# Kernel optimization log

Hardware: AMD Instinct MI355X
Metric: run time of the kernel (lower is better)

Reference implementation:

```python
import jax, jax.numpy as jnp
import numpy as np

K = 3          # kernel size
SH, SW = 2, 1  # stride
PH, PW = 1, 1  # padding


def conv2d(x, w, b, stride, pad):
    y = jax.lax.conv_general_dilated(
        x, w, window_strides=stride,
        padding=[(pad[0], pad[0]), (pad[1], pad[1])],
        dimension_numbers=('NCHW', 'OIHW', 'NCHW'))
    return y + b[None, :, None, None]


def setup_inputs() -> dict:
    key = jax.random.key(0)
    ks = jax.random.split(key, 4)
    x = jax.random.normal(ks[0], (8, 64, 128, 128), jnp.float32)
    # scale offset weights small so sampled offsets are O(1) pixels (exercises
    # the bilinear path without sampling far out of bounds)
    w_offset = jax.random.normal(ks[1], (18, 64, 3, 3), jnp.float32) * 0.02
    b_offset = jnp.zeros((18,), jnp.float32)
    w_mask = jax.random.normal(ks[2], (9, 64, 3, 3), jnp.float32) * 0.05
    b_mask = jnp.zeros((9,), jnp.float32)
    w_conv = jax.random.normal(ks[3], (64, 64, 3, 3), jnp.float32) * (1.0 / 24.0)
    return dict(x=x, w_offset=w_offset, b_offset=b_offset,
                w_mask=w_mask, b_mask=b_mask, w_conv=w_conv)


def _bilinear_gather(x, py, px):
    # x: [B,C,H,W]; py, px: [B,K2,Ho,Wo] float sampling coordinates.
    # Zero-padding outside the image (torchvision deform_conv2d semantics).
    B, C, H, W = x.shape
    y0f = jnp.floor(py)
    x0f = jnp.floor(px)
    dy = py - y0f
    dx = px - x0f
    y0 = y0f.astype(jnp.int32)
    x0 = x0f.astype(jnp.int32)

    def corner(yi, xi, wgt):
        valid = (yi >= 0) & (yi < H) & (xi >= 0) & (xi < W)
        yc = jnp.clip(yi, 0, H - 1)
        xc = jnp.clip(xi, 0, W - 1)
        # per-batch fancy gather -> [B, C, K2, Ho, Wo]
        g = jax.vmap(lambda xb, yb, xbi: xb[:, yb, xbi])(x, yc, xc)
        return g * (wgt * valid)[:, None]

    return (corner(y0,     x0,     (1 - dy) * (1 - dx))
            + corner(y0,     x0 + 1, (1 - dy) * dx)
            + corner(y0 + 1, x0,     dy * (1 - dx))
            + corner(y0 + 1, x0 + 1, dy * dx))


def reference(x, w_offset, b_offset, w_mask, b_mask, w_conv):
    B, C, H, W = x.shape
    offset = conv2d(x, w_offset, b_offset, (SH, SW), (PH, PW))   # [B, 2*K2, Ho, Wo]
    mask = jax.nn.sigmoid(conv2d(x, w_mask, b_mask, (SH, SW), (PH, PW)))  # [B, K2, Ho, Wo]
    Ho, Wo = offset.shape[2], offset.shape[3]
    K2 = K * K
    off = offset.reshape(B, K2, 2, Ho, Wo)
    off_y = off[:, :, 0]   # [B,K2,Ho,Wo]
    off_x = off[:, :, 1]
    ky = (jnp.arange(K2) // K).astype(jnp.float32)
    kx = (jnp.arange(K2) % K).astype(jnp.float32)
    hs = (jnp.arange(Ho) * SH - PH).astype(jnp.float32)
    ws = (jnp.arange(Wo) * SW - PW).astype(jnp.float32)
    py = off_y + ky[None, :, None, None] + hs[None, None, :, None]
    px = off_x + kx[None, :, None, None] + ws[None, None, None, :]
    sampled = _bilinear_gather(x, py, px) * mask[:, None]  # [B,C,K2,Ho,Wo]
    # weighted accumulate over in-channels and kernel taps
    out = jnp.einsum('ock,bckhw->bohw', w_conv.reshape(-1, C, K2), sampled)
    return out
```

## Files before the change

### kernel.cpp

```cpp
#include <hip/hip_runtime.h>
#include <hip/hip_bf16.h>
#include <hip/hip_fp16.h>
#include <math.h>

#define BB 8
#define CC 64
#define HH 128
#define WW 128
#define HO 64
#define WO 128
#define OC 64
#define HW (HH * WW)
#define HOWO (HO * WO)

typedef __attribute__((ext_vector_type(8))) short short8;
typedef __attribute__((ext_vector_type(4))) float floatx4;

union BfBits { __hip_bfloat16 h; unsigned short s; };
__device__ __forceinline__ unsigned short f2bf(float f) {
    BfBits b; b.h = __float2bfloat16(f); return b.s;
}
__device__ __forceinline__ float bflo(unsigned int u) {
    return __uint_as_float(u << 16);
}
__device__ __forceinline__ float bfhi(unsigned int u) {
    return __uint_as_float(u & 0xFFFF0000u);
}

__global__ __launch_bounds__(256) void prep(
    const float* __restrict__ x,
    const float* __restrict__ w_off, const float* __restrict__ w_msk,
    const float* __restrict__ w_conv,
    unsigned short* __restrict__ xT, unsigned int* __restrict__ xP,
    unsigned short* __restrict__ Wom, unsigned short* __restrict__ W2)
{
    __shared__ float T[64][130];
    int tid = threadIdx.x;
    int bx = blockIdx.x;
    if (bx < 1024) {
        int b = bx & 7, y = bx >> 3;
        int wl = tid & 127, c0 = tid >> 7;
#pragma unroll
        for (int i = 0; i < 32; ++i) {
            int c = 2 * i + c0;
            T[c][wl] = x[(((size_t)b * CC + c) * HH + y) * WW + wl];
        }
        __syncthreads();
        int c = tid & 63, wg = tid >> 6;
#pragma unroll
        for (int i = 0; i < 32; ++i) {
            int wp = wg * 32 + i;
            unsigned int lo = f2bf(T[c][wp]);
            unsigned int hi = (wp < 127) ? f2bf(T[c][wp + 1]) : 0u;
            size_t e = (((size_t)b * HH + y) * WW + wp) * 64 + c;
            xT[e] = (unsigned short)lo;
            xP[e] = lo | (hi << 16);
        }
    } else if (bx < 1096) {
        int i = (bx - 1024) * 256 + tid;
        int ch = i / 576, kk = i % 576;
        int xs = kk >> 6, c = kk & 63;
        float v = 0.0f;
        if (ch < 18)      v = w_off[(ch * CC + c) * 9 + xs];
        else if (ch < 27) v = w_msk[((ch - 18) * CC + c) * 9 + xs];
        Wom[i] = f2bf(v);
    } else {
        int i = (bx - 1096) * 256 + tid;
        int k = i % 9, c = (i / 9) % CC, o = i / (CC * 9);
        W2[((size_t)k * OC + o) * CC + c] = f2bf(w_conv[i]);
    }
}

__global__ __launch_bounds__(256) void fused(
    const unsigned short* __restrict__ xT, const unsigned int* __restrict__ xP,
    const unsigned short* __restrict__ Wom, const unsigned short* __restrict__ W2,
    const float* __restrict__ b_off, const float* __restrict__ b_msk,
    float* __restrict__ out)
{
    __shared__ __align__(16) char lds[18304];
    typedef unsigned short XsRow[34][72];
    XsRow* Xs = (XsRow*)lds;
    unsigned short (*S)[32][64] = (unsigned short(*)[32][64])lds;
    uint4* meta = (uint4*)(lds + 8192);
    float (*omr)[33] = (float(*)[33])(lds + 14720);

    int tid = threadIdx.x;
    int lane = tid & 63;
    int wv = __builtin_amdgcn_readfirstlane(tid >> 6);
    int bx = blockIdx.x;
    int b = bx & 7;
    int rest = bx >> 3;
    int h = rest >> 2;
    int w0 = (rest & 3) * 32;
    int h2 = 2 * h - 1;
    int m16 = lane & 15, q = lane >> 4;

    for (int u = tid; u < 816; u += 256) {
        int ky = u / 272;
        int rem = u - ky * 272;
        int col = rem >> 3, cb = rem & 7;
        int hy = h2 + ky, wc = w0 - 1 + col;
        short8 v = {0, 0, 0, 0, 0, 0, 0, 0};
        if ((unsigned)hy < (unsigned)HH && (unsigned)wc < (unsigned)WW)
            v = *(const short8*)(xT + (((size_t)b * HH + hy) * WW + wc) * 64 + cb * 8);
        *(short8*)&Xs[ky][col][cb * 8] = v;
    }
    __syncthreads();

    {
        int mt = wv & 1, nt = wv >> 1;
        floatx4 a = (floatx4){0.f, 0.f, 0.f, 0.f};
        const unsigned short* wa = Wom + (mt * 16 + m16) * 576 + q * 8;
#pragma unroll
        for (int t = 0; t < 18; ++t) {
            int xs = t >> 1, ky = xs / 3, kx = xs % 3;
            short8 af = *(const short8*)(wa + t * 32);
            short8 bf = *(const short8*)&Xs[ky][nt * 16 + m16 + kx][(t & 1) * 32 + q * 8];
            a = __builtin_amdgcn_mfma_f32_16x16x32_bf16(af, bf, a, 0, 0, 0);
        }
#pragma unroll
        for (int r = 0; r < 4; ++r) {
            int ch = mt * 16 + q * 4 + r;
            if (ch < 27) omr[ch][nt * 16 + m16] = a[r];
        }
    }
    __syncthreads();

    for (int u = tid; u < 288; u += 256) {
        int kk = u >> 5, pos = u & 31;
        float offy = omr[2 * kk][pos] + b_off[2 * kk];
        float offx = omr[2 * kk + 1][pos] + b_off[2 * kk + 1];
        float mk = 1.0f / (1.0f + __expf(-(omr[18 + kk][pos] + b_msk[kk])));
        float py = offy + (float)(kk / 3) + (float)h2;
        float px = offx + (float)(kk % 3) + (float)(w0 + pos - 1);

        float y0f = floorf(py), x0f = floorf(px);
        float dy = py - y0f, dx = px - x0f;
        int y0 = (int)y0f, x0 = (int)x0f;
        int y1 = y0 + 1, x1 = x0 + 1;
        bool vy0 = (unsigned)y0 < (unsigned)HH;
        bool vy1 = (unsigned)y1 < (unsigned)HH;
        bool vx0 = (unsigned)x0 < (unsigned)WW;
        bool vx1 = (unsigned)x1 < (unsigned)WW;
        float w00 = (1.0f - dy) * (1.0f - dx) * ((vy0 && vx0) ? mk : 0.0f);
        float w01 = (1.0f - dy) * dx          * ((vy0 && vx1) ? mk : 0.0f);
        float w10 = dy * (1.0f - dx)          * ((vy1 && vx0) ? mk : 0.0f);
        float w11 = dy * dx                   * ((vy1 && vx1) ? mk : 0.0f);
        int xbase = min(max(x0, 0), WW - 2);
        bool s0 = x0 > xbase;
        bool s1 = x1 > xbase;
        float cxA = (s0 ? 0.f : w00) + (s1 ? 0.f : w01);
        float cyA = (s0 ? w00 : 0.f) + (s1 ? w01 : 0.f);
        float cxB = (s0 ? 0.f : w10) + (s1 ? 0.f : w11);
        float cyB = (s0 ? w10 : 0.f) + (s1 ? w11 : 0.f);
        int yc0 = min(max(y0, 0), HH - 1);
        int yc1 = min(max(y1, 0), HH - 1);

        __half2 hA = __floats2half2_rn(cxA, cyA);
        __half2 hB = __floats2half2_rn(cxB, cyB);
        uint4 mu;
        mu.x = __builtin_bit_cast(unsigned int, hA);
        mu.y = __builtin_bit_cast(unsigned int, hB);
        mu.z = (unsigned)(yc0 * WW + xbase) * 256u;
        mu.w = (unsigned)(yc1 * WW + xbase) * 256u;
        meta[u] = mu;
    }
    __syncthreads();

    int p0 = wv * 8;
    int c = lane;
    const char* xPb = (const char*)(xP + (size_t)b * HW * 64);
    floatx4 acc0 = (floatx4){0.f, 0.f, 0.f, 0.f};
    floatx4 acc1 = (floatx4){0.f, 0.f, 0.f, 0.f};

    uint4 M[8];
    unsigned int G0[8], G1[8];

    auto issue = [&](int k) {
#pragma unroll
        for (int i = 0; i < 8; ++i) {
            M[i] = meta[k * 32 + p0 + i];
            G0[i] = *(const unsigned int*)(xPb + M[i].z + 4 * c);
            G1[i] = *(const unsigned int*)(xPb + M[i].w + 4 * c);
        }
    };
    auto store = [&](int buf) {
#pragma unroll
        for (int i = 0; i < 8; ++i) {
            __half2 hA = __builtin_bit_cast(__half2, M[i].x);
            __half2 hB = __builtin_bit_cast(__half2, M[i].y);
            float v = __low2float(hA) * bflo(G0[i]) + __high2float(hA) * bfhi(G0[i])
                    + __low2float(hB) * bflo(G1[i]) + __high2float(hB) * bfhi(G1[i]);
            int pos = p0 + i;
            S[buf][pos][((c >> 3) ^ (pos & 7)) * 8 + (c & 7)] = f2bf(v);
        }
    };

    issue(0);
    store(0);

#pragma unroll
    for (int k = 0; k < 9; ++k) {
        __syncthreads();
        if (k < 8) issue(k + 1);
        {
            const unsigned short* wk = W2 + ((size_t)(k * OC) + wv * 16 + m16) * CC + q * 8;
            int buf = k & 1;
#pragma unroll
            for (int s = 0; s < 2; ++s) {
                short8 af = *(const short8*)(wk + s * 32);
                int cb = ((q + 4 * s) ^ (m16 & 7)) * 8;
                short8 bf0 = *(const short8*)&S[buf][m16][cb];
                short8 bf1 = *(const short8*)&S[buf][16 + m16][cb];
                acc0 = __builtin_amdgcn_mfma_f32_16x16x32_bf16(af, bf0, acc0, 0, 0, 0);
                acc1 = __builtin_amdgcn_mfma_f32_16x16x32_bf16(af, bf1, acc1, 0, 0, 0);
            }
        }
        if (k < 8) store((k + 1) & 1);
    }

#pragma unroll
    for (int nt = 0; nt < 2; ++nt) {
        floatx4 av = nt ? acc1 : acc0;
#pragma unroll
        for (int r = 0; r < 4; ++r) {
            int o = wv * 16 + q * 4 + r;
            out[(((size_t)b * OC + o) * HO + h) * WO + w0 + nt * 16 + m16] = av[r];
        }
    }
}

extern "C" void kernel_launch(void* const* d_in, const int* in_sizes, int n_in,
                              void* d_out, int out_size, void* d_ws, size_t ws_size,
                              hipStream_t stream)
{
    const float* x      = (const float*)d_in[0];
    const float* w_off  = (const float*)d_in[1];
    const float* b_off  = (const float*)d_in[2];
    const float* w_msk  = (const float*)d_in[3];
    const float* b_msk  = (const float*)d_in[4];
    const float* w_conv = (const float*)d_in[5];
    float* out = (float*)d_out;

    unsigned short* xT = (unsigned short*)d_ws;
    unsigned int* xP = (unsigned int*)(xT + (size_t)BB * HW * 64);
    unsigned short* Wom = (unsigned short*)(xP + (size_t)BB * HW * 64);
    unsigned short* W2 = Wom + 32 * 576;

    prep<<<dim3(1240), dim3(256), 0, stream>>>(x, w_off, w_msk, w_conv,
                                               xT, xP, Wom, W2);
    fused<<<dim3(2048), dim3(256), 0, stream>>>(xT, xP, Wom, W2,
                                                b_off, b_msk, out);
}
```

Before: 146.1 us.

## Switch to fp16 packed-pair layout with deeper gather pipelining and scalarized addresses

```diff
diff --git a/kernel.cpp b/kernel.cpp
--- a/kernel.cpp
+++ b/kernel.cpp
@@ -1,5 +1,4 @@
 #include <hip/hip_runtime.h>
-#include <hip/hip_bf16.h>
 #include <hip/hip_fp16.h>
 #include <math.h>
 
@@ -11,77 +10,95 @@
 #define WO 128
 #define OC 64
 #define HW (HH * WW)
-#define HOWO (HO * WO)
-
-typedef __attribute__((ext_vector_type(8))) short short8;
+
 typedef __attribute__((ext_vector_type(4))) float floatx4;
-
-union BfBits { __hip_bfloat16 h; unsigned short s; };
-__device__ __forceinline__ unsigned short f2bf(float f) {
-    BfBits b; b.h = __float2bfloat16(f); return b.s;
-}
-__device__ __forceinline__ float bflo(unsigned int u) {
-    return __uint_as_float(u << 16);
-}
-__device__ __forceinline__ float bfhi(unsigned int u) {
-    return __uint_as_float(u & 0xFFFF0000u);
+typedef __attribute__((ext_vector_type(8))) _Float16 half8;
+
+__device__ __forceinline__ unsigned short f2h(float f) {
+    __half h = __float2half(f);
+    return __builtin_bit_cast(unsigned short, h);
+}
+__device__ __forceinline__ unsigned int packpair(float a, float b) {
+    __half2 h = __floats2half2_rn(a, b);
+    return __builtin_bit_cast(unsigned int, h);
+}
+__device__ __forceinline__ void lgkm_barrier() {
+    asm volatile("s_waitcnt lgkmcnt(0)" ::: "memory");
+    __builtin_amdgcn_s_barrier();
 }
 
 __global__ __launch_bounds__(256) void prep(
     const float* __restrict__ x,
     const float* __restrict__ w_off, const float* __restrict__ w_msk,
     const float* __restrict__ w_conv,
-    unsigned short* __restrict__ xT, unsigned int* __restrict__ xP,
+    unsigned int* __restrict__ xP,
     unsigned short* __restrict__ Wom, unsigned short* __restrict__ W2)
 {
-    __shared__ float T[64][130];
-    int tid = threadIdx.x;
-    int bx = blockIdx.x;
-    if (bx < 1024) {
-        int b = bx & 7, y = bx >> 3;
-        int wl = tid & 127, c0 = tid >> 7;
-#pragma unroll
-        for (int i = 0; i < 32; ++i) {
-            int c = 2 * i + c0;
-            T[c][wl] = x[(((size_t)b * CC + c) * HH + y) * WW + wl];
+    __shared__ float T[64][77];
+    int tid = threadIdx.x, bx = blockIdx.x;
+    if (bx < 2048) {
+        int wh = bx & 1, b = (bx >> 1) & 7, y = bx >> 4;
+        int w0 = wh << 6;
+        const float* xb = x + (((size_t)b * CC) * HH + y) * WW + w0;
+#pragma unroll
+        for (int i = 0; i < 4; ++i) {
+            int idx = i * 256 + tid;
+            int cch = idx >> 4, f4 = (idx & 15) << 2;
+            floatx4 v = *(const floatx4*)(xb + (size_t)cch * HW + f4);
+            T[cch][f4 + 0] = v.x;
+            T[cch][f4 + 1] = v.y;
+            T[cch][f4 + 2] = v.z;
+            T[cch][f4 + 3] = v.w;
+        }
+        if (tid < 64) {
+            float e = 0.0f;
+            if (w0 + 64 < WW) e = xb[(size_t)tid * HW + 64];
+            T[tid][64] = e;
         }
         __syncthreads();
-        int c = tid & 63, wg = tid >> 6;
-#pragma unroll
-        for (int i = 0; i < 32; ++i) {
-            int wp = wg * 32 + i;
-            unsigned int lo = f2bf(T[c][wp]);
-            unsigned int hi = (wp < 127) ? f2bf(T[c][wp + 1]) : 0u;
-            size_t e = (((size_t)b * HH + y) * WW + wp) * 64 + c;
-            xT[e] = (unsigned short)lo;
-            xP[e] = lo | (hi << 16);
-        }
-    } else if (bx < 1096) {
-        int i = (bx - 1024) * 256 + tid;
-        int ch = i / 576, kk = i % 576;
-        int xs = kk >> 6, c = kk & 63;
+        int ch = tid & 63;
+        int wb = (tid >> 6) << 4;
+        size_t base = ((((size_t)b * HH + y) * WW) + w0 + wb) * 64 + ch;
+#pragma unroll
+        for (int j = 0; j < 4; ++j) {
+            int wl = wb + 4 * j;
+            float a0 = T[ch][wl + 0];
+            float a1 = T[ch][wl + 1];
+            float a2 = T[ch][wl + 2];
+            float a3 = T[ch][wl + 3];
+            float a4 = T[ch][wl + 4];
+            xP[base + (size_t)(4 * j + 0) * 64] = packpair(a0, a1);
+            xP[base + (size_t)(4 * j + 1) * 64] = packpair(a1, a2);
+            xP[base + (size_t)(4 * j + 2) * 64] = packpair(a2, a3);
+            xP[base + (size_t)(4 * j + 3) * 64] = packpair(a3, a4);
+        }
+    } else if (bx < 2120) {
+        int i = (bx - 2048) * 256 + tid;
+        int chn = i / 576, kk = i % 576;
+        int xs = kk >> 6, cc = kk & 63;
         float v = 0.0f;
-        if (ch < 18)      v = w_off[(ch * CC + c) * 9 + xs];
-        else if (ch < 27) v = w_msk[((ch - 18) * CC + c) * 9 + xs];
-        Wom[i] = f2bf(v);
+        if (chn < 18)      v = w_off[(chn * CC + cc) * 9 + xs];
+        else if (chn < 27) v = w_msk[((chn - 18) * CC + cc) * 9 + xs];
+        Wom[i] = f2h(v);
     } else {
-        int i = (bx - 1096) * 256 + tid;
-        int k = i % 9, c = (i / 9) % CC, o = i / (CC * 9);
-        W2[((size_t)k * OC + o) * CC + c] = f2bf(w_conv[i]);
-    }
-}
-
-__global__ __launch_bounds__(256) void fused(
-    const unsigned short* __restrict__ xT, const unsigned int* __restrict__ xP,
+        int i = (bx - 2120) * 256 + tid;
+        int k = i % 9, cc = (i / 9) % CC, o = i / (CC * 9);
+        W2[((size_t)k * OC + o) * CC + cc] = f2h(w_conv[i]);
+    }
+}
+
+__global__ __launch_bounds__(256, 8) void fused(
+    const unsigned int* __restrict__ xP,
     const unsigned short* __restrict__ Wom, const unsigned short* __restrict__ W2,
     const float* __restrict__ b_off, const float* __restrict__ b_msk,
     float* __restrict__ out)
 {
     __shared__ __align__(16) char lds[18304];
-    typedef unsigned short XsRow[34][72];
+    typedef _Float16 XsRow[34][72];
     XsRow* Xs = (XsRow*)lds;
     unsigned short (*S)[32][64] = (unsigned short(*)[32][64])lds;
-    uint4* meta = (uint4*)(lds + 8192);
+    uint2* metaC = (uint2*)(lds + 8192);
+    uint2* metaR = (uint2*)(lds + 10496);
     float (*omr)[33] = (float(*)[33])(lds + 14720);
 
     int tid = threadIdx.x;
@@ -95,36 +112,42 @@
     int h2 = 2 * h - 1;
     int m16 = lane & 15, q = lane >> 4;
 
-    for (int u = tid; u < 816; u += 256) {
-        int ky = u / 272;
-        int rem = u - ky * 272;
-        int col = rem >> 3, cb = rem & 7;
+    const unsigned int* xPb_u = xP + (size_t)b * HW * 64;
+
+    for (int u = tid; u < 1632; u += 256) {
+        int ky = u / 544;
+        int rem = u - ky * 544;
+        int col = rem >> 4, c4 = rem & 15;
         int hy = h2 + ky, wc = w0 - 1 + col;
-        short8 v = {0, 0, 0, 0, 0, 0, 0, 0};
-        if ((unsigned)hy < (unsigned)HH && (unsigned)wc < (unsigned)WW)
-            v = *(const short8*)(xT + (((size_t)b * HH + hy) * WW + wc) * 64 + cb * 8);
-        *(short8*)&Xs[ky][col][cb * 8] = v;
-    }
-    __syncthreads();
+        unsigned int lo0 = 0u, lo1 = 0u;
+        if ((unsigned)hy < (unsigned)HH && (unsigned)wc < (unsigned)WW) {
+            const uint4 g = *(const uint4*)(xPb_u + ((size_t)hy * WW + wc) * 64 + c4 * 4);
+            lo0 = (g.x & 0xffffu) | (g.y << 16);
+            lo1 = (g.z & 0xffffu) | (g.w << 16);
+        }
+        uint2* dst = (uint2*)((unsigned short*)lds + ((ky * 34 + col) * 72 + c4 * 4));
+        *dst = make_uint2(lo0, lo1);
+    }
+    lgkm_barrier();
 
     {
         int mt = wv & 1, nt = wv >> 1;
         floatx4 a = (floatx4){0.f, 0.f, 0.f, 0.f};
-        const unsigned short* wa = Wom + (mt * 16 + m16) * 576 + q * 8;
+        const _Float16* wa = (const _Float16*)Wom + (mt * 16 + m16) * 576 + q * 8;
 #pragma unroll
         for (int t = 0; t < 18; ++t) {
             int xs = t >> 1, ky = xs / 3, kx = xs % 3;
-            short8 af = *(const short8*)(wa + t * 32);
-            short8 bf = *(const short8*)&Xs[ky][nt * 16 + m16 + kx][(t & 1) * 32 + q * 8];
-            a = __builtin_amdgcn_mfma_f32_16x16x32_bf16(af, bf, a, 0, 0, 0);
+            half8 af = *(const half8*)(wa + t * 32);
+            half8 bf = *(const half8*)&Xs[ky][nt * 16 + m16 + kx][(t & 1) * 32 + q * 8];
+            a = __builtin_amdgcn_mfma_f32_16x16x32_f16(af, bf, a, 0, 0, 0);
         }
 #pragma unroll
         for (int r = 0; r < 4; ++r) {
-            int ch = mt * 16 + q * 4 + r;
-            if (ch < 27) omr[ch][nt * 16 + m16] = a[r];
-        }
-    }
-    __syncthreads();
+            int chn = mt * 16 + q * 4 + r;
+            if (chn < 27) omr[chn][nt * 16 + m16] = a[r];
+        }
+    }
+    lgkm_barrier();
 
     for (int u = tid; u < 288; u += 256) {
         int kk = u >> 5, pos = u & 31;
@@ -158,65 +181,74 @@
 
         __half2 hA = __floats2half2_rn(cxA, cyA);
         __half2 hB = __floats2half2_rn(cxB, cyB);
-        uint4 mu;
-        mu.x = __builtin_bit_cast(unsigned int, hA);
-        mu.y = __builtin_bit_cast(unsigned int, hB);
-        mu.z = (unsigned)(yc0 * WW + xbase) * 256u;
-        mu.w = (unsigned)(yc1 * WW + xbase) * 256u;
-        meta[u] = mu;
-    }
-    __syncthreads();
+        metaC[u] = make_uint2(__builtin_bit_cast(unsigned int, hA),
+                              __builtin_bit_cast(unsigned int, hB));
+        metaR[u] = make_uint2((unsigned)(yc0 * WW + xbase) * 256u,
+                              (unsigned)(yc1 * WW + xbase) * 256u);
+    }
+    lgkm_barrier();
 
     int p0 = wv * 8;
-    int c = lane;
-    const char* xPb = (const char*)(xP + (size_t)b * HW * 64);
+    const char* xPb = (const char*)xPb_u;
+    unsigned int voff = 4u * (unsigned)lane;
     floatx4 acc0 = (floatx4){0.f, 0.f, 0.f, 0.f};
     floatx4 acc1 = (floatx4){0.f, 0.f, 0.f, 0.f};
 
-    uint4 M[8];
-    unsigned int G0[8], G1[8];
-
-    auto issue = [&](int k) {
+    unsigned int Ga0[8], Ga1[8], Gb0[8], Gb1[8];
+
+    auto issue = [&](int k, unsigned int (&A0)[8], unsigned int (&A1)[8]) {
 #pragma unroll
         for (int i = 0; i < 8; ++i) {
-            M[i] = meta[k * 32 + p0 + i];
-            G0[i] = *(const unsigned int*)(xPb + M[i].z + 4 * c);
-            G1[i] = *(const unsigned int*)(xPb + M[i].w + 4 * c);
+            uint2 zw = metaR[k * 32 + p0 + i];
+            const char* r0 = xPb + (unsigned)__builtin_amdgcn_readfirstlane((int)zw.x);
+            const char* r1 = xPb + (unsigned)__builtin_amdgcn_readfirstlane((int)zw.y);
+            A0[i] = *(const unsigned int*)(r0 + voff);
+            A1[i] = *(const unsigned int*)(r1 + voff);
         }
     };
-    auto store = [&](int buf) {
+    auto dostore = [&](int k, int buf, unsigned int (&A0)[8], unsigned int (&A1)[8]) {
 #pragma unroll
         for (int i = 0; i < 8; ++i) {
-            __half2 hA = __builtin_bit_cast(__half2, M[i].x);
-            __half2 hB = __builtin_bit_cast(__half2, M[i].y);
-            float v = __low2float(hA) * bflo(G0[i]) + __high2float(hA) * bfhi(G0[i])
-                    + __low2float(hB) * bflo(G1[i]) + __high2float(hB) * bfhi(G1[i]);
+            uint2 cf = metaC[k * 32 + p0 + i];
+            __half2 hA = __builtin_bit_cast(__half2, cf.x);
+            __half2 hB = __builtin_bit_cast(__half2, cf.y);
+            __half2 g0 = __builtin_bit_cast(__half2, A0[i]);
+            __half2 g1 = __builtin_bit_cast(__half2, A1[i]);
+            __half2 p = __hfma2(hA, g0, __hmul2(hB, g1));
+            __half sv = __hadd(__low2half(p), __high2half(p));
             int pos = p0 + i;
-            S[buf][pos][((c >> 3) ^ (pos & 7)) * 8 + (c & 7)] = f2bf(v);
+            S[buf][pos][((lane >> 3) ^ (pos & 7)) * 8 + (lane & 7)] =
+                __builtin_bit_cast(unsigned short, sv);
         }
     };
-
-    issue(0);
-    store(0);
-
+    auto mfma_step = [&](int k, int buf) {
+        const _Float16* wk = (const _Float16*)W2
+            + ((size_t)(k * OC) + wv * 16 + m16) * CC + q * 8;
+#pragma unroll
+        for (int s = 0; s < 2; ++s) {
+            half8 af = *(const half8*)(wk + s * 32);
+            int cb = ((q + 4 * s) ^ (m16 & 7)) * 8;
+            half8 bf0 = *(const half8*)&S[buf][m16][cb];
+            half8 bf1 = *(const half8*)&S[buf][16 + m16][cb];
+            acc0 = __builtin_amdgcn_mfma_f32_16x16x32_f16(af, bf0, acc0, 0, 0, 0);
+            acc1 = __builtin_amdgcn_mfma_f32_16x16x32_f16(af, bf1, acc1, 0, 0, 0);
+        }
+    };
+
+    issue(0, Ga0, Ga1);
+    dostore(0, 0, Ga0, Ga1);
+    issue(1, Gb0, Gb1);
 #pragma unroll
     for (int k = 0; k < 9; ++k) {
-        __syncthreads();
-        if (k < 8) issue(k + 1);
-        {
-            const unsigned short* wk = W2 + ((size_t)(k * OC) + wv * 16 + m16) * CC + q * 8;
-            int buf = k & 1;
-#pragma unroll
-            for (int s = 0; s < 2; ++s) {
-                short8 af = *(const short8*)(wk + s * 32);
-                int cb = ((q + 4 * s) ^ (m16 & 7)) * 8;
-                short8 bf0 = *(const short8*)&S[buf][m16][cb];
-                short8 bf1 = *(const short8*)&S[buf][16 + m16][cb];
-                acc0 = __builtin_amdgcn_mfma_f32_16x16x32_bf16(af, bf0, acc0, 0, 0, 0);
-                acc1 = __builtin_amdgcn_mfma_f32_16x16x32_bf16(af, bf1, acc1, 0, 0, 0);
-            }
-        }
-        if (k < 8) store((k + 1) & 1);
+        lgkm_barrier();
+        mfma_step(k, k & 1);
+        if ((k & 1) == 0) {
+            if (k < 7) issue(k + 2, Ga0, Ga1);
+            if (k < 8) dostore(k + 1, (k + 1) & 1, Gb0, Gb1);
+        } else {
+            if (k < 7) issue(k + 2, Gb0, Gb1);
+            if (k < 8) dostore(k + 1, (k + 1) & 1, Ga0, Ga1);
+        }
     }
 
 #pragma unroll
@@ -242,13 +274,12 @@
     const float* w_conv = (const float*)d_in[5];
     float* out = (float*)d_out;
 
-    unsigned short* xT = (unsigned short*)d_ws;
-    unsigned int* xP = (unsigned int*)(xT + (size_t)BB * HW * 64);
+    unsigned int* xP = (unsigned int*)d_ws;
     unsigned short* Wom = (unsigned short*)(xP + (size_t)BB * HW * 64);
     unsigned short* W2 = Wom + 32 * 576;
 
-    prep<<<dim3(1240), dim3(256), 0, stream>>>(x, w_off, w_msk, w_conv,
-                                               xT, xP, Wom, W2);
-    fused<<<dim3(2048), dim3(256), 0, stream>>>(xT, xP, Wom, W2,
+    prep<<<dim3(2264), dim3(256), 0, stream>>>(x, w_off, w_msk, w_conv,
+                                               xP, Wom, W2);
+    fused<<<dim3(2048), dim3(256), 0, stream>>>(xP, Wom, W2,
                                                 b_off, b_msk, out);
 }
```

Result: slower. 155.3 us (+6.3%).
